# Optimization experiments

Measured on AMD Instinct MI355X. Metric: run time of the kernel, lower is better.

## Reference

```python
import jax, jax.numpy as jnp
import numpy as np

NUM_POS = 4
N = 8192
C = 4096  # number of identity classes == logit dim


def setup_inputs() -> dict:
    key = jax.random.key(0)
    k1, k2 = jax.random.split(key)
    feat = jax.random.normal(k1, (N, C), dtype=jnp.float32)
    label = jax.random.randint(k2, (N,), 0, C, dtype=jnp.int64)
    return {"feat": feat, "label": label}


def reference(feat, label):
    # feat: [n, C] logits, label: [n] int class ids.
    n, c = feat.shape
    # Segment-mean replaces the O(n^2) masked-mean loop:
    # center[i] = mean of feat over all j with label[j] == label[i]
    sums = jax.ops.segment_sum(feat, label, num_segments=c)              # [C, C]
    counts = jax.ops.segment_sum(jnp.ones((n,), feat.dtype), label,
                                 num_segments=c)                          # [C]
    center = sums[label] / counts[label][:, None]                         # [n, C]
    # CrossEntropyLoss (mean reduction) on centers as logits
    logp = jax.nn.log_softmax(center, axis=-1)
    ce = -jnp.take_along_axis(logp, label[:, None], axis=1)[:, 0].mean()
    m = n / NUM_POS
    return ce / m
```

## Files before the change

### kernel.cpp

```cpp
#include <hip/hip_runtime.h>
#include <math.h>

#define NN 8192
#define CC 4096
#define SLOTS 64
#define BLK 256
#define NSPLIT 4
#define NF4 (CC / 4)

#define SCALE (4.0f / (8192.0f * 8192.0f))

__global__ void init_kernel(int* __restrict__ counts, float* __restrict__ out) {
    int i = blockIdx.x * blockDim.x + threadIdx.x;
    if (i < CC) counts[i] = 0;
    if (i == 0) out[0] = 0.0f;
}

__global__ void build_index(const int* __restrict__ label,
                            int* __restrict__ counts,
                            int* __restrict__ lists) {
    int i = blockIdx.x * blockDim.x + threadIdx.x;
    if (i < NN) {
        int lab = label[i];
        int pos = atomicAdd(&counts[lab], 1);
        if (pos < SLOTS) lists[lab * SLOTS + pos] = i;
    }
}

template <int T>
__device__ inline void gather4(const float4* __restrict__ feat4,
                               const int* __restrict__ rl, int m,
                               int slot, float4 acc[4]) {
    int r0 = rl[0];
    float4 v[T][4];
    #pragma unroll
    for (int k = 0; k < T; ++k) {
        int r = (k < m) ? rl[k] : r0;
        size_t rb = (size_t)r * NF4 + slot;
        #pragma unroll
        for (int j = 0; j < 4; ++j) v[k][j] = feat4[rb + j * 64];
    }
    #pragma unroll
    for (int k = 0; k < T; ++k) {
        float w = (k < m) ? 1.f : 0.f;
        #pragma unroll
        for (int j = 0; j < 4; ++j) {
            acc[j].x += w * v[k][j].x; acc[j].y += w * v[k][j].y;
            acc[j].z += w * v[k][j].z; acc[j].w += w * v[k][j].w;
        }
    }
}

__global__ __launch_bounds__(BLK) void part_kernel(const float4* __restrict__ feat4,
                                                   const int* __restrict__ counts,
                                                   const int* __restrict__ lists,
                                                   float4* __restrict__ part) {
    int lane = threadIdx.x & 63;
    int wv = __builtin_amdgcn_readfirstlane(threadIdx.x >> 6);
    int task = blockIdx.x * 4 + wv;
    int c = task >> 2;
    int s = task & 3;

    int cnt = counts[c];
    if (cnt == 0) return;
    int m = cnt < SLOTS ? cnt : SLOTS;

    const int* rl = lists + c * SLOTS;
    int slot = s * 256 + lane;

    float4 acc[4];
    #pragma unroll
    for (int j = 0; j < 4; ++j) acc[j] = make_float4(0.f, 0.f, 0.f, 0.f);

    if (m == 1)      gather4<1>(feat4, rl, m, slot, acc);
    else if (m == 2) gather4<2>(feat4, rl, m, slot, acc);
    else if (m <= 4) gather4<4>(feat4, rl, m, slot, acc);
    else {
        gather4<4>(feat4, rl, 4, slot, acc);
        for (int k = 4; k < m; ++k) {
            size_t rb = (size_t)rl[k] * NF4 + slot;
            #pragma unroll
            for (int j = 0; j < 4; ++j) {
                float4 v = feat4[rb + j * 64];
                acc[j].x += v.x; acc[j].y += v.y; acc[j].z += v.z; acc[j].w += v.w;
            }
        }
    }

    float inv = 1.0f / (float)cnt;
    float4 mean[4];
    #pragma unroll
    for (int j = 0; j < 4; ++j) {
        mean[j].x = acc[j].x * inv; mean[j].y = acc[j].y * inv;
        mean[j].z = acc[j].z * inv; mean[j].w = acc[j].w * inv;
    }

    float M = -1e30f;
    #pragma unroll
    for (int j = 0; j < 4; ++j)
        M = fmaxf(M, fmaxf(fmaxf(mean[j].x, mean[j].y), fmaxf(mean[j].z, mean[j].w)));
    #pragma unroll
    for (int off = 1; off < 64; off <<= 1) M = fmaxf(M, __shfl_xor(M, off, 64));

    float S = 0.f;
    #pragma unroll
    for (int j = 0; j < 4; ++j)
        S += __expf(mean[j].x - M) + __expf(mean[j].y - M) +
             __expf(mean[j].z - M) + __expf(mean[j].w - M);
    #pragma unroll
    for (int off = 1; off < 64; off <<= 1) S += __shfl_xor(S, off, 64);

    int sIdx = (c >> 2) & 255;
    int jj = sIdx >> 6, comp = c & 3;
    float cand = 0.f;
    #pragma unroll
    for (int j = 0; j < 4; ++j) {
        cand = (jj == j && comp == 0) ? mean[j].x : cand;
        cand = (jj == j && comp == 1) ? mean[j].y : cand;
        cand = (jj == j && comp == 2) ? mean[j].z : cand;
        cand = (jj == j && comp == 3) ? mean[j].w : cand;
    }
    float vcown = __shfl(cand, sIdx & 63, 64);
    float vc = (s == (c >> 10)) ? vcown : 0.f;

    if (lane == 0) part[s * CC + c] = make_float4(M, S, vc, 0.f);
}

__global__ __launch_bounds__(BLK) void finalize(const float4* __restrict__ part,
                                                const int* __restrict__ counts,
                                                float* __restrict__ out) {
    int c = blockIdx.x * BLK + threadIdx.x;
    int cnt = counts[c];
    float contrib = 0.f;
    if (cnt > 0) {
        float4 p[NSPLIT];
        #pragma unroll
        for (int s = 0; s < NSPLIT; ++s) p[s] = part[s * CC + c];
        float M = p[0].x;
        #pragma unroll
        for (int s = 1; s < NSPLIT; ++s) M = fmaxf(M, p[s].x);
        float S = 0.f, vc = 0.f;
        #pragma unroll
        for (int s = 0; s < NSPLIT; ++s) {
            S += p[s].y * __expf(p[s].x - M);
            vc += p[s].z;
        }
        contrib = (float)cnt * (M + __logf(S) - vc);
    }

    #pragma unroll
    for (int off = 1; off < 64; off <<= 1) contrib += __shfl_xor(contrib, off, 64);
    __shared__ float s_red[4];
    int lane = threadIdx.x & 63, w = threadIdx.x >> 6;
    if (lane == 0) s_red[w] = contrib;
    __syncthreads();
    if (threadIdx.x == 0)
        atomicAdd(out, (s_red[0] + s_red[1] + s_red[2] + s_red[3]) * SCALE);
}

extern "C" void kernel_launch(void* const* d_in, const int* in_sizes, int n_in,
                              void* d_out, int out_size, void* d_ws, size_t ws_size,
                              hipStream_t stream) {
    const float* feat = (const float*)d_in[0];
    const int* label = (const int*)d_in[1];
    float* out = (float*)d_out;

    int* counts = (int*)d_ws;
    int* lists = counts + CC;
    float4* part = (float4*)(lists + CC * SLOTS);

    init_kernel<<<(CC + BLK - 1) / BLK, BLK, 0, stream>>>(counts, out);
    build_index<<<(NN + BLK - 1) / BLK, BLK, 0, stream>>>(label, counts, lists);
    part_kernel<<<CC * NSPLIT / 4, BLK, 0, stream>>>((const float4*)feat, counts, lists, part);
    finalize<<<CC / BLK, BLK, 0, stream>>>(part, counts, out);
}
```

Before: 201.1 us.

## Fuse index build and finalize into fewer kernels with last-block reduction

Replaces the init and global-atomic index build kernels with a single one-block kernel that counts labels in shared memory, and folds the finalize kernel into the part kernel. Each block now handles one class across its four waves, merges the split softmax stats through shared memory, and the last block to finish (detected with an atomic counter) does the final sum. This removes two kernel launches and the partial-results round trip. The cost is a serial single-block build over all labels and a threadfence/atomic per block.

```diff
diff --git a/kernel.cpp b/kernel.cpp
--- a/kernel.cpp
+++ b/kernel.cpp
@@ -10,21 +10,25 @@
 
 #define SCALE (4.0f / (8192.0f * 8192.0f))
 
-__global__ void init_kernel(int* __restrict__ counts, float* __restrict__ out) {
-    int i = blockIdx.x * blockDim.x + threadIdx.x;
-    if (i < CC) counts[i] = 0;
-    if (i == 0) out[0] = 0.0f;
-}
-
-__global__ void build_index(const int* __restrict__ label,
-                            int* __restrict__ counts,
-                            int* __restrict__ lists) {
-    int i = blockIdx.x * blockDim.x + threadIdx.x;
-    if (i < NN) {
+__global__ __launch_bounds__(1024) void build_kernel(const int* __restrict__ label,
+                                                     int* __restrict__ counts,
+                                                     int* __restrict__ lists,
+                                                     unsigned* __restrict__ done) {
+    __shared__ int s_cnt[CC];
+    int t = threadIdx.x;
+    #pragma unroll
+    for (int i = t; i < CC; i += 1024) s_cnt[i] = 0;
+    if (t == 0) *done = 0u;
+    __syncthreads();
+    #pragma unroll
+    for (int i = t; i < NN; i += 1024) {
         int lab = label[i];
-        int pos = atomicAdd(&counts[lab], 1);
+        int pos = atomicAdd(&s_cnt[lab], 1);
         if (pos < SLOTS) lists[lab * SLOTS + pos] = i;
     }
+    __syncthreads();
+    #pragma unroll
+    for (int i = t; i < CC; i += 1024) counts[i] = s_cnt[i];
 }
 
 template <int T>
@@ -54,108 +58,118 @@
 __global__ __launch_bounds__(BLK) void part_kernel(const float4* __restrict__ feat4,
                                                    const int* __restrict__ counts,
                                                    const int* __restrict__ lists,
-                                                   float4* __restrict__ part) {
-    int lane = threadIdx.x & 63;
-    int wv = __builtin_amdgcn_readfirstlane(threadIdx.x >> 6);
-    int task = blockIdx.x * 4 + wv;
-    int c = task >> 2;
-    int s = task & 3;
+                                                   float* __restrict__ contrib,
+                                                   unsigned* __restrict__ done,
+                                                   float* __restrict__ out) {
+    int t = threadIdx.x;
+    int lane = t & 63;
+    int s = __builtin_amdgcn_readfirstlane(t >> 6);
+    int c = blockIdx.x;
+
+    __shared__ float s_m[NSPLIT], s_s[NSPLIT], s_v[NSPLIT];
+    __shared__ int s_last;
 
     int cnt = counts[c];
-    if (cnt == 0) return;
-    int m = cnt < SLOTS ? cnt : SLOTS;
+    if (cnt > 0) {
+        int m = cnt < SLOTS ? cnt : SLOTS;
+        const int* rl = lists + c * SLOTS;
+        int slot = s * 256 + lane;
 
-    const int* rl = lists + c * SLOTS;
-    int slot = s * 256 + lane;
+        float4 acc[4];
+        #pragma unroll
+        for (int j = 0; j < 4; ++j) acc[j] = make_float4(0.f, 0.f, 0.f, 0.f);
 
-    float4 acc[4];
-    #pragma unroll
-    for (int j = 0; j < 4; ++j) acc[j] = make_float4(0.f, 0.f, 0.f, 0.f);
-
-    if (m == 1)      gather4<1>(feat4, rl, m, slot, acc);
-    else if (m == 2) gather4<2>(feat4, rl, m, slot, acc);
-    else if (m <= 4) gather4<4>(feat4, rl, m, slot, acc);
-    else {
-        gather4<4>(feat4, rl, 4, slot, acc);
-        for (int k = 4; k < m; ++k) {
-            size_t rb = (size_t)rl[k] * NF4 + slot;
-            #pragma unroll
-            for (int j = 0; j < 4; ++j) {
-                float4 v = feat4[rb + j * 64];
-                acc[j].x += v.x; acc[j].y += v.y; acc[j].z += v.z; acc[j].w += v.w;
+        if (m == 1)      gather4<1>(feat4, rl, m, slot, acc);
+        else if (m == 2) gather4<2>(feat4, rl, m, slot, acc);
+        else if (m <= 4) gather4<4>(feat4, rl, m, slot, acc);
+        else {
+            gather4<4>(feat4, rl, 4, slot, acc);
+            for (int k = 4; k < m; ++k) {
+                size_t rb = (size_t)rl[k] * NF4 + slot;
+                #pragma unroll
+                for (int j = 0; j < 4; ++j) {
+                    float4 v = feat4[rb + j * 64];
+                    acc[j].x += v.x; acc[j].y += v.y; acc[j].z += v.z; acc[j].w += v.w;
+                }
             }
         }
+
+        float inv = 1.0f / (float)cnt;
+        float4 mean[4];
+        #pragma unroll
+        for (int j = 0; j < 4; ++j) {
+            mean[j].x = acc[j].x * inv; mean[j].y = acc[j].y * inv;
+            mean[j].z = acc[j].z * inv; mean[j].w = acc[j].w * inv;
+        }
+
+        float M = -1e30f;
+        #pragma unroll
+        for (int j = 0; j < 4; ++j)
+            M = fmaxf(M, fmaxf(fmaxf(mean[j].x, mean[j].y), fmaxf(mean[j].z, mean[j].w)));
+        #pragma unroll
+        for (int off = 1; off < 64; off <<= 1) M = fmaxf(M, __shfl_xor(M, off, 64));
+
+        float S = 0.f;
+        #pragma unroll
+        for (int j = 0; j < 4; ++j)
+            S += __expf(mean[j].x - M) + __expf(mean[j].y - M) +
+                 __expf(mean[j].z - M) + __expf(mean[j].w - M);
+        #pragma unroll
+        for (int off = 1; off < 64; off <<= 1) S += __shfl_xor(S, off, 64);
+
+        int sIdx = (c >> 2) & 255;
+        int jj = sIdx >> 6, comp = c & 3;
+        float cand = 0.f;
+        #pragma unroll
+        for (int j = 0; j < 4; ++j) {
+            cand = (jj == j && comp == 0) ? mean[j].x : cand;
+            cand = (jj == j && comp == 1) ? mean[j].y : cand;
+            cand = (jj == j && comp == 2) ? mean[j].z : cand;
+            cand = (jj == j && comp == 3) ? mean[j].w : cand;
+        }
+        float vcown = __shfl(cand, sIdx & 63, 64);
+        float vc = (s == (c >> 10)) ? vcown : 0.f;
+
+        if (lane == 0) { s_m[s] = M; s_s[s] = S; s_v[s] = vc; }
     }
+    __syncthreads();
 
-    float inv = 1.0f / (float)cnt;
-    float4 mean[4];
-    #pragma unroll
-    for (int j = 0; j < 4; ++j) {
-        mean[j].x = acc[j].x * inv; mean[j].y = acc[j].y * inv;
-        mean[j].z = acc[j].z * inv; mean[j].w = acc[j].w * inv;
+    if (t == 0) {
+        if (cnt > 0) {
+            float M = s_m[0];
+            #pragma unroll
+            for (int j = 1; j < NSPLIT; ++j) M = fmaxf(M, s_m[j]);
+            float S = 0.f, vc = 0.f;
+            #pragma unroll
+            for (int j = 0; j < NSPLIT; ++j) {
+                S += s_s[j] * __expf(s_m[j] - M);
+                vc += s_v[j];
+            }
+            contrib[c] = (float)cnt * (M + __logf(S) - vc);
+        }
+        __threadfence();
+        unsigned old = atomicAdd(done, 1u);
+        s_last = (old == (unsigned)(gridDim.x - 1)) ? 1 : 0;
     }
+    __syncthreads();
 
-    float M = -1e30f;
-    #pragma unroll
-    for (int j = 0; j < 4; ++j)
-        M = fmaxf(M, fmaxf(fmaxf(mean[j].x, mean[j].y), fmaxf(mean[j].z, mean[j].w)));
-    #pragma unroll
-    for (int off = 1; off < 64; off <<= 1) M = fmaxf(M, __shfl_xor(M, off, 64));
-
-    float S = 0.f;
-    #pragma unroll
-    for (int j = 0; j < 4; ++j)
-        S += __expf(mean[j].x - M) + __expf(mean[j].y - M) +
-             __expf(mean[j].z - M) + __expf(mean[j].w - M);
-    #pragma unroll
-    for (int off = 1; off < 64; off <<= 1) S += __shfl_xor(S, off, 64);
-
-    int sIdx = (c >> 2) & 255;
-    int jj = sIdx >> 6, comp = c & 3;
-    float cand = 0.f;
-    #pragma unroll
-    for (int j = 0; j < 4; ++j) {
-        cand = (jj == j && comp == 0) ? mean[j].x : cand;
-        cand = (jj == j && comp == 1) ? mean[j].y : cand;
-        cand = (jj == j && comp == 2) ? mean[j].z : cand;
-        cand = (jj == j && comp == 3) ? mean[j].w : cand;
+    if (s_last) {
+        __threadfence();
+        float sum = 0.f;
+        for (int i = t; i < CC; i += BLK) {
+            int cn = counts[i];
+            if (cn > 0)
+                sum += __hip_atomic_load(&contrib[i], __ATOMIC_RELAXED,
+                                         __HIP_MEMORY_SCOPE_AGENT);
+        }
+        #pragma unroll
+        for (int off = 1; off < 64; off <<= 1) sum += __shfl_xor(sum, off, 64);
+        __shared__ float s_red[4];
+        if (lane == 0) s_red[t >> 6] = sum;
+        __syncthreads();
+        if (t == 0)
+            out[0] = (s_red[0] + s_red[1] + s_red[2] + s_red[3]) * SCALE;
     }
-    float vcown = __shfl(cand, sIdx & 63, 64);
-    float vc = (s == (c >> 10)) ? vcown : 0.f;
-
-    if (lane == 0) part[s * CC + c] = make_float4(M, S, vc, 0.f);
-}
-
-__global__ __launch_bounds__(BLK) void finalize(const float4* __restrict__ part,
-                                                const int* __restrict__ counts,
-                                                float* __restrict__ out) {
-    int c = blockIdx.x * BLK + threadIdx.x;
-    int cnt = counts[c];
-    float contrib = 0.f;
-    if (cnt > 0) {
-        float4 p[NSPLIT];
-        #pragma unroll
-        for (int s = 0; s < NSPLIT; ++s) p[s] = part[s * CC + c];
-        float M = p[0].x;
-        #pragma unroll
-        for (int s = 1; s < NSPLIT; ++s) M = fmaxf(M, p[s].x);
-        float S = 0.f, vc = 0.f;
-        #pragma unroll
-        for (int s = 0; s < NSPLIT; ++s) {
-            S += p[s].y * __expf(p[s].x - M);
-            vc += p[s].z;
-        }
-        contrib = (float)cnt * (M + __logf(S) - vc);
-    }
-
-    #pragma unroll
-    for (int off = 1; off < 64; off <<= 1) contrib += __shfl_xor(contrib, off, 64);
-    __shared__ float s_red[4];
-    int lane = threadIdx.x & 63, w = threadIdx.x >> 6;
-    if (lane == 0) s_red[w] = contrib;
-    __syncthreads();
-    if (threadIdx.x == 0)
-        atomicAdd(out, (s_red[0] + s_red[1] + s_red[2] + s_red[3]) * SCALE);
 }
 
 extern "C" void kernel_launch(void* const* d_in, const int* in_sizes, int n_in,
@@ -167,10 +181,10 @@
 
     int* counts = (int*)d_ws;
     int* lists = counts + CC;
-    float4* part = (float4*)(lists + CC * SLOTS);
+    float* contrib = (float*)(lists + CC * SLOTS);
+    unsigned* done = (unsigned*)(contrib + CC);
 
-    init_kernel<<<(CC + BLK - 1) / BLK, BLK, 0, stream>>>(counts, out);
-    build_index<<<(NN + BLK - 1) / BLK, BLK, 0, stream>>>(label, counts, lists);
-    part_kernel<<<CC * NSPLIT / 4, BLK, 0, stream>>>((const float4*)feat, counts, lists, part);
-    finalize<<<CC / BLK, BLK, 0, stream>>>(part, counts, out);
+    build_kernel<<<1, 1024, 0, stream>>>(label, counts, lists, done);
+    part_kernel<<<CC, BLK, 0, stream>>>((const float4*)feat, counts, lists,
+                                        contrib, done, out);
 }
```

Result: slower. 402.8 us (+100.3%).
